# Kernel optimization log

Hardware: AMD Instinct MI355X
Metric: run time of the kernel (lower is better)

## Reference

```python
import jax, jax.numpy as jnp
import numpy as np

EPS = 1e-8

def _center(G):
    # Double-centering: H @ G @ H with H = I - 11^T/n, expressed as mean subtraction.
    # Identical math to the torch H-matmul version, O(n^2) instead of O(n^3).
    row = jnp.mean(G, axis=-1, keepdims=True)
    col = jnp.mean(G, axis=-2, keepdims=True)
    tot = jnp.mean(G, axis=(-2, -1), keepdims=True)
    return G - row - col + tot


def setup_inputs() -> dict:
    key = jax.random.key(0)
    k1, k2 = jax.random.split(key)
    B, L, H, M = 32, 128, 512, 512
    x = jax.random.normal(k1, (B, L, H), dtype=jnp.float32)
    # nn.Embedding.from_pretrained(torch.normal(-0.01, 0.2, (M, L*H)))
    centroid_w = jax.random.normal(k2, (M, L * H), dtype=jnp.float32) * 0.2 - 0.01
    return {"x": x, "centroid_w": centroid_w}


def reference(x, centroid_w):
    B, L, H = x.shape
    M = centroid_w.shape[0]
    cent = centroid_w.reshape(M, L, H)

    # Centered linear Grams
    Cx = _center(jnp.einsum('blh,bkh->blk', x, x))        # (B, L, L)
    Cy = _center(jnp.einsum('mlh,mkh->mlk', cent, cent))  # (M, L, L)

    # linear HSIC: sum over LxL of elementwise product -> (B, M)
    hsic = jnp.einsum('bij,mij->bm', Cx, Cy)
    vx = jnp.sqrt(jnp.sum(Cx * Cx, axis=(1, 2)))  # (B,)  sqrt(HSIC(x,x))
    vy = jnp.sqrt(jnp.sum(Cy * Cy, axis=(1, 2)))  # (M,)  sqrt(HSIC(y,y))
    cka_loss_matrix = -jnp.log(jnp.abs(hsic / (vx[:, None] * vy[None, :])) + EPS)

    idx = jnp.argmax(cka_loss_matrix, axis=-1)  # (B,)
    sel = cent[idx]                              # (B, L, H) gathered centroids

    # Second CKA pass against selected centroids; torch broadcasting makes (B, B)
    Cs = _center(jnp.einsum('blh,bkh->blk', sel, sel))  # (B, L, L)
    hsic2 = jnp.einsum('bij,cij->bc', Cx, Cs)           # (B, B)
    vs = jnp.sqrt(jnp.sum(Cs * Cs, axis=(1, 2)))        # (B,)
    cka_loss = -jnp.log(jnp.mean(jnp.abs(hsic2 / (vx[:, None] * vs[None, :]))) + EPS)

    return cka_loss, cka_loss_matrix, idx
```

## Files before the change

kernel.cpp:

```cpp
#include <hip/hip_runtime.h>
#include <math.h>

#define BB 32
#define LL 128
#define HH 512
#define MM 512
#define NM 544
#define EPSF 1e-8f
#define CPLEN 10240
#define NCH 40

typedef __attribute__((ext_vector_type(8))) short short8b;
typedef __attribute__((ext_vector_type(4))) float f32x4;
typedef __attribute__((ext_vector_type(16))) float f32x16;

#define NWS_CP    0
#define NWS_PART  5570560
#define NWS_NSQ   6225920
#define NWS_HSIC  6226464
#define NWS_IDS   6242848

__device__ __forceinline__ unsigned pack2(unsigned lo, unsigned hi) {
    return (lo >> 16) | (hi & 0xffff0000u);
}

__device__ __forceinline__ void split3(const float4 lo, const float4 hi,
                                       uint4& p0, uint4& p1, uint4& p2) {
    float c[8] = {lo.x, lo.y, lo.z, lo.w, hi.x, hi.y, hi.z, hi.w};
    unsigned h[8], m[8], l[8];
#pragma unroll
    for (int i = 0; i < 8; ++i) {
        h[i] = __float_as_uint(c[i]) & 0xffff0000u;
        const float r1 = c[i] - __uint_as_float(h[i]);
        m[i] = __float_as_uint(r1) & 0xffff0000u;
        l[i] = __float_as_uint(r1 - __uint_as_float(m[i]));
    }
    p0 = make_uint4(pack2(h[0],h[1]), pack2(h[2],h[3]), pack2(h[4],h[5]), pack2(h[6],h[7]));
    p1 = make_uint4(pack2(m[0],m[1]), pack2(m[2],m[3]), pack2(m[4],m[5]), pack2(m[6],m[7]));
    p2 = make_uint4(pack2(l[0],l[1]), pack2(l[2],l[3]), pack2(l[4],l[5]), pack2(l[6],l[7]));
}

__device__ __forceinline__ f32x16 mfma6(f32x16 d, const short8b a[3], const short8b b[3]) {
    d = __builtin_amdgcn_mfma_f32_32x32x16_bf16(a[0], b[0], d, 0, 0, 0);
    d = __builtin_amdgcn_mfma_f32_32x32x16_bf16(a[0], b[1], d, 0, 0, 0);
    d = __builtin_amdgcn_mfma_f32_32x32x16_bf16(a[1], b[0], d, 0, 0, 0);
    d = __builtin_amdgcn_mfma_f32_32x32x16_bf16(a[1], b[1], d, 0, 0, 0);
    d = __builtin_amdgcn_mfma_f32_32x32x16_bf16(a[0], b[2], d, 0, 0, 0);
    d = __builtin_amdgcn_mfma_f32_32x32x16_bf16(a[2], b[0], d, 0, 0, 0);
    return d;
}

__device__ __forceinline__ void ldstrip(const uint4* P, int strip, int lane, short8b f[3]) {
    const int s = lane >> 5;
    const int r = strip * 32 + (lane & 31);
#pragma unroll
    for (int p = 0; p < 3; ++p) {
        uint4 u = P[(p * 2 + s) * 128 + r];
        f[p] = *(const short8b*)&u;
    }
}

__device__ __forceinline__ void tile_sums(f32x16 a, float* S, int i, int j,
                                          bool offd, int lane) {
    const int hi = lane >> 5;
    float rs[16];
#pragma unroll
    for (int q = 0; q < 16; ++q) {
        float s = a[q];
        s += __shfl_xor(s, 1, 64);
        s += __shfl_xor(s, 2, 64);
        s += __shfl_xor(s, 4, 64);
        s += __shfl_xor(s, 8, 64);
        s += __shfl_xor(s, 16, 64);
        rs[q] = s;
    }
    if ((lane & 31) == 0) {
#pragma unroll
        for (int q = 0; q < 16; ++q)
            S[i * 32 + (q & 3) + 8 * (q >> 2) + 4 * hi] += rs[q];
    }
    if (offd) {
        float cs = 0.f;
#pragma unroll
        for (int q = 0; q < 16; ++q) cs += a[q];
        cs += __shfl_xor(cs, 32, 64);
        if (lane < 32) S[j * 32 + lane] += cs;
    }
}

__device__ __forceinline__ float tile_fin(f32x16 a, const float* rmv, float gm,
                                          bool offd, int i, int j,
                                          float* dst, int lane) {
    const int hi = lane >> 5, col = lane & 31;
    const float cj = rmv[j * 32 + col];
    const float sc = offd ? 1.41421356237309505f : 1.f;
    float nsq = 0.f;
#pragma unroll
    for (int c = 0; c < 4; ++c) {
        const float4 ri = *(const float4*)&rmv[i * 32 + c * 8 + hi * 4];
        const float riq[4] = {ri.x, ri.y, ri.z, ri.w};
        f32x4 o;
#pragma unroll
        for (int q = 0; q < 4; ++q) {
            float vq = (a[c * 4 + q] + gm - riq[q] - cj) * sc;
            nsq = fmaf(vq, vq, nsq);
            o[q] = vq;
        }
        *(f32x4*)(dst + (c * 2 + hi) * 128 + col * 4) = o;
    }
    return nsq;
}

__global__ __launch_bounds__(256, 4)
void gram_sym2(const float* __restrict__ x,
               const float* __restrict__ cent,
               float* __restrict__ Cp,
               float* __restrict__ normsq)
{
    __shared__ uint4 planes[2][3][2][128];
    __shared__ float Ssh[4][128];
    __shared__ float rmv[128];
    __shared__ float red[256];
    __shared__ float gmsh;

    const int tid  = threadIdx.x;
    const int lane = tid & 63;
    const int wid  = tid >> 6;
    const int n    = blockIdx.x;
    const float* Amat = (n < BB) ? (x + (size_t)n * LL * HH)
                                 : (cent + (size_t)(n - BB) * LL * HH);

    const int srow  = tid >> 1;
    const int shalf = tid & 1;

    f32x16 a0, a1, a2;
#pragma unroll
    for (int q = 0; q < 16; ++q) { a0[q] = 0.f; a1[q] = 0.f; a2[q] = 0.f; }

    float4 v0 = *(const float4*)(Amat + (size_t)srow * HH + shalf * 8);
    float4 v1 = *(const float4*)(Amat + (size_t)srow * HH + shalf * 8 + 4);

    for (int t = 0; t < 32; ++t) {
        const int pb = t & 1;
        uint4 p0, p1, p2;
        split3(v0, v1, p0, p1, p2);
        uint4* P = &planes[pb][0][0][0];
        const int wbase = shalf * 128 + srow;
        P[0 * 256 + wbase] = p0;
        P[1 * 256 + wbase] = p1;
        P[2 * 256 + wbase] = p2;

        const int kn = (t < 31) ? (t + 1) * 16 : 496;
        v0 = *(const float4*)(Amat + (size_t)srow * HH + kn + shalf * 8);
        v1 = *(const float4*)(Amat + (size_t)srow * HH + kn + shalf * 8 + 4);

        __syncthreads();

        const uint4* Pr = &planes[pb][0][0][0];
        short8b fa[3], fb[3];
        if (wid == 0) {
            ldstrip(Pr, 3, lane, fb);
            ldstrip(Pr, 0, lane, fa); a0 = mfma6(a0, fa, fb);
            ldstrip(Pr, 1, lane, fa); a1 = mfma6(a1, fa, fb);
            ldstrip(Pr, 2, lane, fa); a2 = mfma6(a2, fa, fb);
        } else if (wid == 1) {
            ldstrip(Pr, 3, lane, fa); a0 = mfma6(a0, fa, fa);
            ldstrip(Pr, 2, lane, fb);
            ldstrip(Pr, 0, lane, fa); a1 = mfma6(a1, fa, fb);
            ldstrip(Pr, 1, lane, fa); a2 = mfma6(a2, fa, fb);
        } else if (wid == 2) {
            ldstrip(Pr, 2, lane, fa); a0 = mfma6(a0, fa, fa);
            ldstrip(Pr, 0, lane, fa);
            ldstrip(Pr, 1, lane, fb); a1 = mfma6(a1, fa, fb);
        } else {
            ldstrip(Pr, 0, lane, fa); a0 = mfma6(a0, fa, fa);
            ldstrip(Pr, 1, lane, fa); a1 = mfma6(a1, fa, fa);
        }
    }

    Ssh[wid][lane] = 0.f;
    Ssh[wid][lane + 64] = 0.f;
    if (wid == 0) {
        tile_sums(a0, Ssh[0], 0, 3, true, lane);
        tile_sums(a1, Ssh[0], 1, 3, true, lane);
        tile_sums(a2, Ssh[0], 2, 3, true, lane);
    } else if (wid == 1) {
        tile_sums(a0, Ssh[1], 3, 3, false, lane);
        tile_sums(a1, Ssh[1], 0, 2, true, lane);
        tile_sums(a2, Ssh[1], 1, 2, true, lane);
    } else if (wid == 2) {
        tile_sums(a0, Ssh[2], 2, 2, false, lane);
        tile_sums(a1, Ssh[2], 0, 1, true, lane);
    } else {
        tile_sums(a0, Ssh[3], 0, 0, false, lane);
        tile_sums(a1, Ssh[3], 1, 1, false, lane);
    }
    __syncthreads();

    float Sv = 0.f;
    if (tid < 128) {
        Sv = Ssh[0][tid] + Ssh[1][tid] + Ssh[2][tid] + Ssh[3][tid];
        rmv[tid] = Sv * (1.f / 128.f);
    }
    red[tid] = (tid < 128) ? Sv : 0.f;
    __syncthreads();
    for (int s2 = 128; s2 > 0; s2 >>= 1) {
        if (tid < s2) red[tid] += red[tid + s2];
        __syncthreads();
    }
    if (tid == 0) gmsh = red[0] * (1.f / 16384.f);
    __syncthreads();
    const float gm = gmsh;

    float nsq = 0.f;
    float* dst = Cp + (size_t)n * CPLEN;
    if (wid == 0) {
        nsq += tile_fin(a0, rmv, gm, true, 0, 3, dst + 3 * 1024, lane);
        nsq += tile_fin(a1, rmv, gm, true, 1, 3, dst + 6 * 1024, lane);
        nsq += tile_fin(a2, rmv, gm, true, 2, 3, dst + 8 * 1024, lane);
    } else if (wid == 1) {
        nsq += tile_fin(a0, rmv, gm, false, 3, 3, dst + 9 * 1024, lane);
        nsq += tile_fin(a1, rmv, gm, true, 0, 2, dst + 2 * 1024, lane);
        nsq += tile_fin(a2, rmv, gm, true, 1, 2, dst + 5 * 1024, lane);
    } else if (wid == 2) {
        nsq += tile_fin(a0, rmv, gm, false, 2, 2, dst + 7 * 1024, lane);
        nsq += tile_fin(a1, rmv, gm, true, 0, 1, dst + 1 * 1024, lane);
    } else {
        nsq += tile_fin(a0, rmv, gm, false, 0, 0, dst + 0 * 1024, lane);
        nsq += tile_fin(a1, rmv, gm, false, 1, 1, dst + 4 * 1024, lane);
    }
    __syncthreads();
    red[tid] = nsq;
    __syncthreads();
    for (int s2 = 128; s2 > 0; s2 >>= 1) {
        if (tid < s2) red[tid] += red[tid + s2];
        __syncthreads();
    }
    if (tid == 0) normsq[n] = red[0];
}

__global__ __launch_bounds__(256, 2)
void hsic_partial(const float* __restrict__ Cp, float* __restrict__ part)
{
    __shared__ float cx[32][260];
    __shared__ float red2[256][16];

    const int tid = threadIdx.x;
    const int bx  = blockIdx.x;
    const int mt  = bx / NCH;
    const int kc  = bx % NCH;
    const int k0  = kc * 256;

#pragma unroll
    for (int i = 0; i < 8; ++i) {
        const int idx = i * 1024 + tid * 4;
        const int b = idx >> 8, k = idx & 255;
        *(float4*)&cx[b][k] = *(const float4*)&Cp[(size_t)b * CPLEN + k0 + k];
    }
    __syncthreads();

    const int kq = tid >> 6;
    const int bg = (tid >> 3) & 7;
    const int mg = tid & 7;
    const float* cyBase = Cp + (size_t)(BB + mt * 32 + mg * 4) * CPLEN + k0 + kq * 64;

    float a[4][4];
#pragma unroll
    for (int bi = 0; bi < 4; ++bi)
#pragma unroll
        for (int mi = 0; mi < 4; ++mi) a[bi][mi] = 0.f;

    for (int kk = 0; kk < 16; ++kk) {
        float4 cy[4];
#pragma unroll
        for (int mi = 0; mi < 4; ++mi)
            cy[mi] = *(const float4*)(cyBase + (size_t)mi * CPLEN + kk * 4);
        float4 cxv[4];
#pragma unroll
        for (int bi = 0; bi < 4; ++bi)
            cxv[bi] = *(const float4*)&cx[bg + bi * 8][kq * 64 + kk * 4];
#pragma unroll
        for (int bi = 0; bi < 4; ++bi)
#pragma unroll
            for (int mi = 0; mi < 4; ++mi) {
                a[bi][mi] = fmaf(cxv[bi].x, cy[mi].x, a[bi][mi]);
                a[bi][mi] = fmaf(cxv[bi].y, cy[mi].y, a[bi][mi]);
                a[bi][mi] = fmaf(cxv[bi].z, cy[mi].z, a[bi][mi]);
                a[bi][mi] = fmaf(cxv[bi].w, cy[mi].w, a[bi][mi]);
            }
    }

#pragma unroll
    for (int e = 0; e < 16; ++e) red2[tid][e] = a[e >> 2][e & 3];
    __syncthreads();
    if (tid < 64) {
#pragma unroll
        for (int e = 0; e < 16; ++e) {
            const float s = red2[tid][e] + red2[tid + 64][e] +
                            red2[tid + 128][e] + red2[tid + 192][e];
            const int bi = e >> 2, mi = e & 3;
            const int b = ((tid >> 3) & 7) + bi * 8;
            const int m = mt * 32 + (tid & 7) * 4 + mi;
            part[((size_t)kc * 32 + b) * 512 + m] = s;
        }
    }
}

__global__ __launch_bounds__(256)
void combine_loss(const float* __restrict__ part,
                  const float* __restrict__ normsq,
                  float* __restrict__ hsic,
                  int* __restrict__ ids,
                  float* __restrict__ out)
{
    __shared__ float rv[256];
    __shared__ int   ri[256];
    const int b = blockIdx.x;
    const int tid = threadIdx.x;
    const float vx = sqrtf(normsq[b]);

    float best = -INFINITY; int bm = 0;
    for (int m = tid; m < MM; m += 256) {
        float s = 0.f;
        for (int kc = 0; kc < NCH; ++kc)
            s += part[((size_t)kc * 32 + b) * 512 + m];
        hsic[b * MM + m] = s;
        const float vy = sqrtf(normsq[BB + m]);
        const float loss = -logf(fabsf(s) / (vx * vy) + EPSF);
        out[1 + b * MM + m] = loss;
        if (loss > best) { best = loss; bm = m; }
    }
    rv[tid] = best; ri[tid] = bm;
    __syncthreads();
    for (int s2 = 128; s2 > 0; s2 >>= 1) {
        if (tid < s2) {
            if (rv[tid + s2] > rv[tid] ||
                (rv[tid + s2] == rv[tid] && ri[tid + s2] < ri[tid])) {
                rv[tid] = rv[tid + s2]; ri[tid] = ri[tid + s2];
            }
        }
        __syncthreads();
    }
    if (tid == 0) { ids[b] = ri[0]; out[1 + BB * MM + b] = (float)ri[0]; }
}

__global__ __launch_bounds__(1024)
void scalar_loss(const float* __restrict__ hsic,
                 const float* __restrict__ normsq,
                 const int* __restrict__ ids,
                 float* __restrict__ out)
{
    __shared__ float red[1024];
    const int tid = threadIdx.x;
    const int b = tid >> 5, c = tid & 31;
    const int m = ids[c];
    red[tid] = fabsf(hsic[b * MM + m]) /
               (sqrtf(normsq[b]) * sqrtf(normsq[BB + m]));
    __syncthreads();
    for (int s = 512; s > 0; s >>= 1) {
        if (tid < s) red[tid] += red[tid + s];
        __syncthreads();
    }
    if (tid == 0) out[0] = -logf(red[0] * (1.f / 1024.f) + EPSF);
}

extern "C" void kernel_launch(void* const* d_in, const int* in_sizes, int n_in,
                              void* d_out, int out_size, void* d_ws, size_t ws_size,
                              hipStream_t stream) {
    const float* x    = (const float*)d_in[0];
    const float* cent = (const float*)d_in[1];
    float* out = (float*)d_out;
    float* ws  = (float*)d_ws;

    float* Cp     = ws + NWS_CP;
    float* part   = ws + NWS_PART;
    float* normsq = ws + NWS_NSQ;
    float* hsic   = ws + NWS_HSIC;
    int*   ids    = (int*)(ws + NWS_IDS);

    gram_sym2<<<NM, 256, 0, stream>>>(x, cent, Cp, normsq);
    hsic_partial<<<16 * NCH, 256, 0, stream>>>(Cp, part);
    combine_loss<<<BB, 256, 0, stream>>>(part, normsq, hsic, ids, out);
    scalar_loss<<<1, 1024, 0, stream>>>(hsic, normsq, ids, out);
}
```

Baseline: 89.42 us.

## Split Gram K-dimension across warps with private staging, reduce tiles in LDS

Each of the four warps now owns a quarter of the hidden dimension and computes all ten upper-triangular 32x32 tiles of the Gram matrix for that slice, staging its own split-bf16 planes in private shared memory. This removes the per-step block-wide __syncthreads and the uneven tile-to-warp assignment of the old kernel. The partial tiles are then summed through shared memory in four serialized rounds, and row sums and centering are computed from that buffer. In exchange it needs 160 accumulator registers per lane, which is why launch bounds drop to two blocks per SIMD, and it adds an LDS reduction phase.

Result: slower. 98.05 us (+9.7%).

```diff
diff --git a/kernel.cpp b/kernel.cpp
--- a/kernel.cpp
+++ b/kernel.cpp
@@ -40,85 +40,33 @@
     p2 = make_uint4(pack2(l[0],l[1]), pack2(l[2],l[3]), pack2(l[4],l[5]), pack2(l[6],l[7]));
 }
 
-__device__ __forceinline__ f32x16 mfma6(f32x16 d, const short8b a[3], const short8b b[3]) {
+__device__ __forceinline__ void mfma6(f32x16& d, const short8b a[3], const short8b b[3]) {
     d = __builtin_amdgcn_mfma_f32_32x32x16_bf16(a[0], b[0], d, 0, 0, 0);
     d = __builtin_amdgcn_mfma_f32_32x32x16_bf16(a[0], b[1], d, 0, 0, 0);
     d = __builtin_amdgcn_mfma_f32_32x32x16_bf16(a[1], b[0], d, 0, 0, 0);
     d = __builtin_amdgcn_mfma_f32_32x32x16_bf16(a[1], b[1], d, 0, 0, 0);
     d = __builtin_amdgcn_mfma_f32_32x32x16_bf16(a[0], b[2], d, 0, 0, 0);
     d = __builtin_amdgcn_mfma_f32_32x32x16_bf16(a[2], b[0], d, 0, 0, 0);
-    return d;
-}
-
-__device__ __forceinline__ void ldstrip(const uint4* P, int strip, int lane, short8b f[3]) {
-    const int s = lane >> 5;
-    const int r = strip * 32 + (lane & 31);
-#pragma unroll
-    for (int p = 0; p < 3; ++p) {
-        uint4 u = P[(p * 2 + s) * 128 + r];
-        f[p] = *(const short8b*)&u;
-    }
-}
-
-__device__ __forceinline__ void tile_sums(f32x16 a, float* S, int i, int j,
-                                          bool offd, int lane) {
-    const int hi = lane >> 5;
-    float rs[16];
-#pragma unroll
-    for (int q = 0; q < 16; ++q) {
-        float s = a[q];
-        s += __shfl_xor(s, 1, 64);
-        s += __shfl_xor(s, 2, 64);
-        s += __shfl_xor(s, 4, 64);
-        s += __shfl_xor(s, 8, 64);
-        s += __shfl_xor(s, 16, 64);
-        rs[q] = s;
-    }
-    if ((lane & 31) == 0) {
-#pragma unroll
-        for (int q = 0; q < 16; ++q)
-            S[i * 32 + (q & 3) + 8 * (q >> 2) + 4 * hi] += rs[q];
-    }
-    if (offd) {
-        float cs = 0.f;
-#pragma unroll
-        for (int q = 0; q < 16; ++q) cs += a[q];
-        cs += __shfl_xor(cs, 32, 64);
-        if (lane < 32) S[j * 32 + lane] += cs;
-    }
-}
-
-__device__ __forceinline__ float tile_fin(f32x16 a, const float* rmv, float gm,
-                                          bool offd, int i, int j,
-                                          float* dst, int lane) {
-    const int hi = lane >> 5, col = lane & 31;
-    const float cj = rmv[j * 32 + col];
-    const float sc = offd ? 1.41421356237309505f : 1.f;
-    float nsq = 0.f;
-#pragma unroll
-    for (int c = 0; c < 4; ++c) {
-        const float4 ri = *(const float4*)&rmv[i * 32 + c * 8 + hi * 4];
-        const float riq[4] = {ri.x, ri.y, ri.z, ri.w};
-        f32x4 o;
-#pragma unroll
-        for (int q = 0; q < 4; ++q) {
-            float vq = (a[c * 4 + q] + gm - riq[q] - cj) * sc;
-            nsq = fmaf(vq, vq, nsq);
-            o[q] = vq;
-        }
-        *(f32x4*)(dst + (c * 2 + hi) * 128 + col * 4) = o;
-    }
-    return nsq;
-}
-
-__global__ __launch_bounds__(256, 4)
-void gram_sym2(const float* __restrict__ x,
-               const float* __restrict__ cent,
-               float* __restrict__ Cp,
-               float* __restrict__ normsq)
+}
+
+__device__ __forceinline__ int flatAB(int a, int b) {
+    return ((a >> 3) * 2 + ((a >> 2) & 1)) * 128 + b * 4 + (a & 3);
+}
+
+__device__ __forceinline__ int Tix(int i, int j) {
+    return i * (7 - i) / 2 + j;
+}
+
+__global__ __launch_bounds__(256, 2)
+void gram_nb(const float* __restrict__ x,
+             const float* __restrict__ cent,
+             float* __restrict__ Cp,
+             float* __restrict__ normsq)
 {
-    __shared__ uint4 planes[2][3][2][128];
-    __shared__ float Ssh[4][128];
+    __shared__ union {
+        uint4 stage[4][3][2][128];
+        float buf[12288];
+    } sm;
     __shared__ float rmv[128];
     __shared__ float red[256];
     __shared__ float gmsh;
@@ -130,79 +78,111 @@
     const float* Amat = (n < BB) ? (x + (size_t)n * LL * HH)
                                  : (cent + (size_t)(n - BB) * LL * HH);
 
-    const int srow  = tid >> 1;
-    const int shalf = tid & 1;
-
-    f32x16 a0, a1, a2;
-#pragma unroll
-    for (int q = 0; q < 16; ++q) { a0[q] = 0.f; a1[q] = 0.f; a2[q] = 0.f; }
-
-    float4 v0 = *(const float4*)(Amat + (size_t)srow * HH + shalf * 8);
-    float4 v1 = *(const float4*)(Amat + (size_t)srow * HH + shalf * 8 + 4);
-
-    for (int t = 0; t < 32; ++t) {
-        const int pb = t & 1;
-        uint4 p0, p1, p2;
-        split3(v0, v1, p0, p1, p2);
-        uint4* P = &planes[pb][0][0][0];
-        const int wbase = shalf * 128 + srow;
-        P[0 * 256 + wbase] = p0;
-        P[1 * 256 + wbase] = p1;
-        P[2 * 256 + wbase] = p2;
-
-        const int kn = (t < 31) ? (t + 1) * 16 : 496;
-        v0 = *(const float4*)(Amat + (size_t)srow * HH + kn + shalf * 8);
-        v1 = *(const float4*)(Amat + (size_t)srow * HH + kn + shalf * 8 + 4);
-
-        __syncthreads();
-
-        const uint4* Pr = &planes[pb][0][0][0];
-        short8b fa[3], fb[3];
-        if (wid == 0) {
-            ldstrip(Pr, 3, lane, fb);
-            ldstrip(Pr, 0, lane, fa); a0 = mfma6(a0, fa, fb);
-            ldstrip(Pr, 1, lane, fa); a1 = mfma6(a1, fa, fb);
-            ldstrip(Pr, 2, lane, fa); a2 = mfma6(a2, fa, fb);
-        } else if (wid == 1) {
-            ldstrip(Pr, 3, lane, fa); a0 = mfma6(a0, fa, fa);
-            ldstrip(Pr, 2, lane, fb);
-            ldstrip(Pr, 0, lane, fa); a1 = mfma6(a1, fa, fb);
-            ldstrip(Pr, 1, lane, fa); a2 = mfma6(a2, fa, fb);
-        } else if (wid == 2) {
-            ldstrip(Pr, 2, lane, fa); a0 = mfma6(a0, fa, fa);
-            ldstrip(Pr, 0, lane, fa);
-            ldstrip(Pr, 1, lane, fb); a1 = mfma6(a1, fa, fb);
-        } else {
-            ldstrip(Pr, 0, lane, fa); a0 = mfma6(a0, fa, fa);
-            ldstrip(Pr, 1, lane, fa); a1 = mfma6(a1, fa, fa);
-        }
-    }
-
-    Ssh[wid][lane] = 0.f;
-    Ssh[wid][lane + 64] = 0.f;
-    if (wid == 0) {
-        tile_sums(a0, Ssh[0], 0, 3, true, lane);
-        tile_sums(a1, Ssh[0], 1, 3, true, lane);
-        tile_sums(a2, Ssh[0], 2, 3, true, lane);
-    } else if (wid == 1) {
-        tile_sums(a0, Ssh[1], 3, 3, false, lane);
-        tile_sums(a1, Ssh[1], 0, 2, true, lane);
-        tile_sums(a2, Ssh[1], 1, 2, true, lane);
-    } else if (wid == 2) {
-        tile_sums(a0, Ssh[2], 2, 2, false, lane);
-        tile_sums(a1, Ssh[2], 0, 1, true, lane);
-    } else {
-        tile_sums(a0, Ssh[3], 0, 0, false, lane);
-        tile_sums(a1, Ssh[3], 1, 1, false, lane);
-    }
-    __syncthreads();
-
-    float Sv = 0.f;
+    const int o   = lane & 1;
+    const int r2  = lane >> 1;
+    const int kw  = wid * 128;
+
+    f32x16 acc[10];
+#pragma unroll
+    for (int g = 0; g < 10; ++g)
+#pragma unroll
+        for (int q = 0; q < 16; ++q) acc[g][q] = 0.f;
+
+    uint4* SW = &sm.stage[wid][0][0][0];
+
+    float4 v0[4], v1[4];
+#pragma unroll
+    for (int p = 0; p < 4; ++p) {
+        const float* rp = Amat + (size_t)(32 * p + r2) * HH + kw + o * 8;
+        v0[p] = *(const float4*)rp;
+        v1[p] = *(const float4*)(rp + 4);
+    }
+
+    for (int t = 0; t < 8; ++t) {
+#pragma unroll
+        for (int p = 0; p < 4; ++p) {
+            uint4 q0, q1, q2;
+            split3(v0[p], v1[p], q0, q1, q2);
+            const int r = 32 * p + r2;
+            SW[(0 * 2 + o) * 128 + r] = q0;
+            SW[(1 * 2 + o) * 128 + r] = q1;
+            SW[(2 * 2 + o) * 128 + r] = q2;
+        }
+        const int kn = kw + ((t < 7) ? (t + 1) * 16 : 112);
+#pragma unroll
+        for (int p = 0; p < 4; ++p) {
+            const float* rp = Amat + (size_t)(32 * p + r2) * HH + kn + o * 8;
+            v0[p] = *(const float4*)rp;
+            v1[p] = *(const float4*)(rp + 4);
+        }
+        const int fo = lane >> 5, frr = lane & 31;
+        short8b fr[4][3];
+#pragma unroll
+        for (int s = 0; s < 4; ++s)
+#pragma unroll
+            for (int pl = 0; pl < 3; ++pl) {
+                uint4 u = SW[(pl * 2 + fo) * 128 + s * 32 + frr];
+                fr[s][pl] = *(const short8b*)&u;
+            }
+        mfma6(acc[0], fr[0], fr[0]);
+        mfma6(acc[1], fr[0], fr[1]);
+        mfma6(acc[4], fr[1], fr[1]);
+        mfma6(acc[2], fr[0], fr[2]);
+        mfma6(acc[5], fr[1], fr[2]);
+        mfma6(acc[7], fr[2], fr[2]);
+        mfma6(acc[3], fr[0], fr[3]);
+        mfma6(acc[6], fr[1], fr[3]);
+        mfma6(acc[8], fr[2], fr[3]);
+        mfma6(acc[9], fr[3], fr[3]);
+    }
+
+    __syncthreads();
+
+    const int hi  = lane >> 5, col = lane & 31;
+#pragma unroll
+    for (int w = 0; w < 4; ++w) {
+        if (wid == w) {
+#pragma unroll
+            for (int g = 0; g < 10; ++g)
+#pragma unroll
+                for (int c = 0; c < 4; ++c) {
+                    const int idx = g * 1024 + (c * 2 + hi) * 128 + col * 4;
+                    f32x4 a4;
+                    a4[0] = acc[g][c * 4 + 0];
+                    a4[1] = acc[g][c * 4 + 1];
+                    a4[2] = acc[g][c * 4 + 2];
+                    a4[3] = acc[g][c * 4 + 3];
+                    if (w > 0) {
+                        const f32x4 old = *(const f32x4*)&sm.buf[idx];
+                        a4[0] += old[0]; a4[1] += old[1];
+                        a4[2] += old[2]; a4[3] += old[3];
+                    }
+                    *(f32x4*)&sm.buf[idx] = a4;
+                }
+        }
+        __syncthreads();
+    }
+
+    float s = 0.f;
     if (tid < 128) {
-        Sv = Ssh[0][tid] + Ssh[1][tid] + Ssh[2][tid] + Ssh[3][tid];
-        rmv[tid] = Sv * (1.f / 128.f);
-    }
-    red[tid] = (tid < 128) ? Sv : 0.f;
+        const int i = tid >> 5, ri = tid & 31;
+#pragma unroll
+        for (int j = 0; j < 4; ++j) {
+            if (j >= i) {
+                const int g = Tix(i, j);
+#pragma unroll
+                for (int b = 0; b < 32; ++b)
+                    s += sm.buf[g * 1024 + flatAB(ri, b)];
+            } else {
+                const int g = Tix(j, i);
+#pragma unroll
+                for (int a = 0; a < 32; ++a)
+                    s += sm.buf[g * 1024 + flatAB(a, ri)];
+            }
+        }
+        rmv[tid] = s * (1.f / 128.f);
+    }
+    red[tid] = (tid < 128) ? s : 0.f;
     __syncthreads();
     for (int s2 = 128; s2 > 0; s2 >>= 1) {
         if (tid < s2) red[tid] += red[tid + s2];
@@ -212,22 +192,29 @@
     __syncthreads();
     const float gm = gmsh;
 
+    const int b  = tid & 31;
+    const int c2 = tid >> 5;
+    const int ar = (c2 >> 1) * 8 + (c2 & 1) * 4;
     float nsq = 0.f;
-    float* dst = Cp + (size_t)n * CPLEN;
-    if (wid == 0) {
-        nsq += tile_fin(a0, rmv, gm, true, 0, 3, dst + 3 * 1024, lane);
-        nsq += tile_fin(a1, rmv, gm, true, 1, 3, dst + 6 * 1024, lane);
-        nsq += tile_fin(a2, rmv, gm, true, 2, 3, dst + 8 * 1024, lane);
-    } else if (wid == 1) {
-        nsq += tile_fin(a0, rmv, gm, false, 3, 3, dst + 9 * 1024, lane);
-        nsq += tile_fin(a1, rmv, gm, true, 0, 2, dst + 2 * 1024, lane);
-        nsq += tile_fin(a2, rmv, gm, true, 1, 2, dst + 5 * 1024, lane);
-    } else if (wid == 2) {
-        nsq += tile_fin(a0, rmv, gm, false, 2, 2, dst + 7 * 1024, lane);
-        nsq += tile_fin(a1, rmv, gm, true, 0, 1, dst + 1 * 1024, lane);
-    } else {
-        nsq += tile_fin(a0, rmv, gm, false, 0, 0, dst + 0 * 1024, lane);
-        nsq += tile_fin(a1, rmv, gm, false, 1, 1, dst + 4 * 1024, lane);
+    float* dstn = Cp + (size_t)n * CPLEN;
+    static const int TI[10] = {0,0,0,0,1,1,1,2,2,3};
+    static const int TJ[10] = {0,1,2,3,1,2,3,2,3,3};
+#pragma unroll
+    for (int g = 0; g < 10; ++g) {
+        const int i = TI[g], j = TJ[g];
+        const float sc = (i == j) ? 1.f : 1.41421356237309505f;
+        const f32x4 vv = *(const f32x4*)&sm.buf[g * 1024 + tid * 4];
+        const float4 rr = *(const float4*)&rmv[i * 32 + ar];
+        const float riq[4] = {rr.x, rr.y, rr.z, rr.w};
+        const float cj = rmv[j * 32 + b];
+        f32x4 ov;
+#pragma unroll
+        for (int q = 0; q < 4; ++q) {
+            const float val = (vv[q] + gm - riq[q] - cj) * sc;
+            nsq = fmaf(val, val, nsq);
+            ov[q] = val;
+        }
+        *(f32x4*)(dstn + g * 1024 + tid * 4) = ov;
     }
     __syncthreads();
     red[tid] = nsq;
@@ -378,7 +365,7 @@
     float* hsic   = ws + NWS_HSIC;
     int*   ids    = (int*)(ws + NWS_IDS);
 
-    gram_sym2<<<NM, 256, 0, stream>>>(x, cent, Cp, normsq);
+    gram_nb<<<NM, 256, 0, stream>>>(x, cent, Cp, normsq);
     hsic_partial<<<16 * NCH, 256, 0, stream>>>(Cp, part);
     combine_loss<<<BB, 256, 0, stream>>>(part, normsq, hsic, ids, out);
     scalar_loss<<<1, 1024, 0, stream>>>(hsic, normsq, ids, out);
```

## Load gram strips per wave directly and center only x grams

Applied to the files above, without the earlier changes.

Each wave now loads its own row strips straight from global memory into registers, splits them into bf16x3 parts and issues MFMAs with no LDS staging and no per-step block barriers. Centroid grams are stored uncentered. Their centered squared norm comes from row sums (sum of squares minus a row-sum correction plus a total-sum term), and a small new kernel centers only the 32 x grams. This relies on a centered Cx making the HSIC inner product the same whether or not Cy is centered. In exchange, strips shared by several waves are loaded and split several times, and occupancy bounds drop from 4 to 2 blocks. The norm formula also subtracts large terms, which can lose float precision.

Result: slower. 122.6 us (+37.1%).

```diff
diff --git a/kernel.cpp b/kernel.cpp
--- a/kernel.cpp
+++ b/kernel.cpp
@@ -9,6 +9,7 @@
 #define EPSF 1e-8f
 #define CPLEN 10240
 #define NCH 40
+#define R2C 1.41421356237309505f
 
 typedef __attribute__((ext_vector_type(8))) short short8b;
 typedef __attribute__((ext_vector_type(4))) float f32x4;
@@ -19,6 +20,7 @@
 #define NWS_NSQ   6225920
 #define NWS_HSIC  6226464
 #define NWS_IDS   6242848
+#define NWS_U     6242880
 
 __device__ __forceinline__ unsigned pack2(unsigned lo, unsigned hi) {
     return (lo >> 16) | (hi & 0xffff0000u);
@@ -40,24 +42,17 @@
     p2 = make_uint4(pack2(l[0],l[1]), pack2(l[2],l[3]), pack2(l[4],l[5]), pack2(l[6],l[7]));
 }
 
-__device__ __forceinline__ f32x16 mfma6(f32x16 d, const short8b a[3], const short8b b[3]) {
+__device__ __forceinline__ void mfma6(f32x16& d, const short8b a[3], const short8b b[3]) {
     d = __builtin_amdgcn_mfma_f32_32x32x16_bf16(a[0], b[0], d, 0, 0, 0);
     d = __builtin_amdgcn_mfma_f32_32x32x16_bf16(a[0], b[1], d, 0, 0, 0);
     d = __builtin_amdgcn_mfma_f32_32x32x16_bf16(a[1], b[0], d, 0, 0, 0);
     d = __builtin_amdgcn_mfma_f32_32x32x16_bf16(a[1], b[1], d, 0, 0, 0);
     d = __builtin_amdgcn_mfma_f32_32x32x16_bf16(a[0], b[2], d, 0, 0, 0);
     d = __builtin_amdgcn_mfma_f32_32x32x16_bf16(a[2], b[0], d, 0, 0, 0);
-    return d;
-}
-
-__device__ __forceinline__ void ldstrip(const uint4* P, int strip, int lane, short8b f[3]) {
-    const int s = lane >> 5;
-    const int r = strip * 32 + (lane & 31);
-#pragma unroll
-    for (int p = 0; p < 3; ++p) {
-        uint4 u = P[(p * 2 + s) * 128 + r];
-        f[p] = *(const short8b*)&u;
-    }
+}
+
+__device__ __forceinline__ constexpr int Tix(int i, int j) {
+    return i * (7 - i) / 2 + j;
 }
 
 __device__ __forceinline__ void tile_sums(f32x16 a, float* S, int i, int j,
@@ -88,155 +83,211 @@
     }
 }
 
-__device__ __forceinline__ float tile_fin(f32x16 a, const float* rmv, float gm,
-                                          bool offd, int i, int j,
-                                          float* dst, int lane) {
-    const int hi = lane >> 5, col = lane & 31;
-    const float cj = rmv[j * 32 + col];
-    const float sc = offd ? 1.41421356237309505f : 1.f;
+__device__ __forceinline__ float tile_store(const f32x16& a, float* dst,
+                                            bool offd, int lane) {
+    const int oct = lane >> 5, col = lane & 31;
+    const float sc = offd ? R2C : 1.f;
     float nsq = 0.f;
 #pragma unroll
     for (int c = 0; c < 4; ++c) {
-        const float4 ri = *(const float4*)&rmv[i * 32 + c * 8 + hi * 4];
-        const float riq[4] = {ri.x, ri.y, ri.z, ri.w};
         f32x4 o;
 #pragma unroll
         for (int q = 0; q < 4; ++q) {
-            float vq = (a[c * 4 + q] + gm - riq[q] - cj) * sc;
-            nsq = fmaf(vq, vq, nsq);
-            o[q] = vq;
-        }
-        *(f32x4*)(dst + (c * 2 + hi) * 128 + col * 4) = o;
+            const float v = a[c * 4 + q] * sc;
+            nsq = fmaf(v, v, nsq);
+            o[q] = v;
+        }
+        *(f32x4*)(dst + (c * 2 + oct) * 128 + col * 4) = o;
     }
     return nsq;
 }
 
-__global__ __launch_bounds__(256, 4)
-void gram_sym2(const float* __restrict__ x,
-               const float* __restrict__ cent,
-               float* __restrict__ Cp,
-               float* __restrict__ normsq)
-{
-    __shared__ uint4 planes[2][3][2][128];
+template<int NS, int NT, int S0, int S1, int S2, int S3,
+         int A0, int B0, int A1, int B1, int A2, int B2>
+__device__ __forceinline__ float wave_gram(const float* __restrict__ Amat,
+                                           float* __restrict__ Sslice,
+                                           float* __restrict__ dstn,
+                                           int lane)
+{
+    const int r31 = lane & 31, oct = lane >> 5;
+    const int SS[4] = {S0, S1, S2, S3};
+
+    Sslice[lane] = 0.f;
+    Sslice[lane + 64] = 0.f;
+
+    const float* base[4];
+#pragma unroll
+    for (int s = 0; s < NS; ++s)
+        base[s] = Amat + (size_t)(SS[s] * 32 + r31) * HH + oct * 8;
+
+    f32x16 t0, t1, t2;
+#pragma unroll
+    for (int q = 0; q < 16; ++q) { t0[q] = 0.f; t1[q] = 0.f; t2[q] = 0.f; }
+
+    float4 cur[4][2], nxt[4][2];
+#pragma unroll
+    for (int s = 0; s < NS; ++s) {
+        cur[s][0] = *(const float4*)(base[s]);
+        cur[s][1] = *(const float4*)(base[s] + 4);
+    }
+
+#pragma unroll 1
+    for (int tt = 0; tt < 16; ++tt) {
+#pragma unroll
+        for (int s = 0; s < NS; ++s) {
+            const float* p = base[s] + (2 * tt + 1) * 16;
+            nxt[s][0] = *(const float4*)p;
+            nxt[s][1] = *(const float4*)(p + 4);
+        }
+        {
+            short8b fr[4][3];
+#pragma unroll
+            for (int s = 0; s < NS; ++s) {
+                uint4 u0, u1, u2;
+                split3(cur[s][0], cur[s][1], u0, u1, u2);
+                fr[s][0] = *(short8b*)&u0;
+                fr[s][1] = *(short8b*)&u1;
+                fr[s][2] = *(short8b*)&u2;
+            }
+            mfma6(t0, fr[A0], fr[B0]);
+            if (NT > 1) mfma6(t1, fr[A1], fr[B1]);
+            if (NT > 2) mfma6(t2, fr[A2], fr[B2]);
+        }
+        if (tt < 15) {
+#pragma unroll
+            for (int s = 0; s < NS; ++s) {
+                const float* p = base[s] + (2 * tt + 2) * 16;
+                cur[s][0] = *(const float4*)p;
+                cur[s][1] = *(const float4*)(p + 4);
+            }
+        }
+        {
+            short8b fr[4][3];
+#pragma unroll
+            for (int s = 0; s < NS; ++s) {
+                uint4 u0, u1, u2;
+                split3(nxt[s][0], nxt[s][1], u0, u1, u2);
+                fr[s][0] = *(short8b*)&u0;
+                fr[s][1] = *(short8b*)&u1;
+                fr[s][2] = *(short8b*)&u2;
+            }
+            mfma6(t0, fr[A0], fr[B0]);
+            if (NT > 1) mfma6(t1, fr[A1], fr[B1]);
+            if (NT > 2) mfma6(t2, fr[A2], fr[B2]);
+        }
+    }
+
+    tile_sums(t0, Sslice, SS[A0], SS[B0], SS[A0] != SS[B0], lane);
+    if (NT > 1) tile_sums(t1, Sslice, SS[A1], SS[B1], SS[A1] != SS[B1], lane);
+    if (NT > 2) tile_sums(t2, Sslice, SS[A2], SS[B2], SS[A2] != SS[B2], lane);
+
+    float nsq = tile_store(t0, dstn + Tix(SS[A0], SS[B0]) * 1024,
+                           SS[A0] != SS[B0], lane);
+    if (NT > 1) nsq += tile_store(t1, dstn + Tix(SS[A1], SS[B1]) * 1024,
+                                  SS[A1] != SS[B1], lane);
+    if (NT > 2) nsq += tile_store(t2, dstn + Tix(SS[A2], SS[B2]) * 1024,
+                                  SS[A2] != SS[B2], lane);
+    return nsq;
+}
+
+__global__ __launch_bounds__(256, 2)
+void gram_direct(const float* __restrict__ x,
+                 const float* __restrict__ cent,
+                 float* __restrict__ Cp,
+                 float* __restrict__ normsq,
+                 float* __restrict__ uws)
+{
     __shared__ float Ssh[4][128];
-    __shared__ float rmv[128];
     __shared__ float red[256];
-    __shared__ float gmsh;
-
-    const int tid  = threadIdx.x;
-    const int lane = tid & 63;
-    const int wid  = tid >> 6;
-    const int n    = blockIdx.x;
+    __shared__ float sS, sUsq;
+
+    const int tid = threadIdx.x, lane = tid & 63, wid = tid >> 6;
+    const int n = blockIdx.x;
     const float* Amat = (n < BB) ? (x + (size_t)n * LL * HH)
                                  : (cent + (size_t)(n - BB) * LL * HH);
-
-    const int srow  = tid >> 1;
-    const int shalf = tid & 1;
-
-    f32x16 a0, a1, a2;
-#pragma unroll
-    for (int q = 0; q < 16; ++q) { a0[q] = 0.f; a1[q] = 0.f; a2[q] = 0.f; }
-
-    float4 v0 = *(const float4*)(Amat + (size_t)srow * HH + shalf * 8);
-    float4 v1 = *(const float4*)(Amat + (size_t)srow * HH + shalf * 8 + 4);
-
-    for (int t = 0; t < 32; ++t) {
-        const int pb = t & 1;
-        uint4 p0, p1, p2;
-        split3(v0, v1, p0, p1, p2);
-        uint4* P = &planes[pb][0][0][0];
-        const int wbase = shalf * 128 + srow;
-        P[0 * 256 + wbase] = p0;
-        P[1 * 256 + wbase] = p1;
-        P[2 * 256 + wbase] = p2;
-
-        const int kn = (t < 31) ? (t + 1) * 16 : 496;
-        v0 = *(const float4*)(Amat + (size_t)srow * HH + kn + shalf * 8);
-        v1 = *(const float4*)(Amat + (size_t)srow * HH + kn + shalf * 8 + 4);
-
-        __syncthreads();
-
-        const uint4* Pr = &planes[pb][0][0][0];
-        short8b fa[3], fb[3];
-        if (wid == 0) {
-            ldstrip(Pr, 3, lane, fb);
-            ldstrip(Pr, 0, lane, fa); a0 = mfma6(a0, fa, fb);
-            ldstrip(Pr, 1, lane, fa); a1 = mfma6(a1, fa, fb);
-            ldstrip(Pr, 2, lane, fa); a2 = mfma6(a2, fa, fb);
-        } else if (wid == 1) {
-            ldstrip(Pr, 3, lane, fa); a0 = mfma6(a0, fa, fa);
-            ldstrip(Pr, 2, lane, fb);
-            ldstrip(Pr, 0, lane, fa); a1 = mfma6(a1, fa, fb);
-            ldstrip(Pr, 1, lane, fa); a2 = mfma6(a2, fa, fb);
-        } else if (wid == 2) {
-            ldstrip(Pr, 2, lane, fa); a0 = mfma6(a0, fa, fa);
-            ldstrip(Pr, 0, lane, fa);
-            ldstrip(Pr, 1, lane, fb); a1 = mfma6(a1, fa, fb);
-        } else {
-            ldstrip(Pr, 0, lane, fa); a0 = mfma6(a0, fa, fa);
-            ldstrip(Pr, 1, lane, fa); a1 = mfma6(a1, fa, fa);
-        }
-    }
-
-    Ssh[wid][lane] = 0.f;
-    Ssh[wid][lane + 64] = 0.f;
-    if (wid == 0) {
-        tile_sums(a0, Ssh[0], 0, 3, true, lane);
-        tile_sums(a1, Ssh[0], 1, 3, true, lane);
-        tile_sums(a2, Ssh[0], 2, 3, true, lane);
-    } else if (wid == 1) {
-        tile_sums(a0, Ssh[1], 3, 3, false, lane);
-        tile_sums(a1, Ssh[1], 0, 2, true, lane);
-        tile_sums(a2, Ssh[1], 1, 2, true, lane);
-    } else if (wid == 2) {
-        tile_sums(a0, Ssh[2], 2, 2, false, lane);
-        tile_sums(a1, Ssh[2], 0, 1, true, lane);
-    } else {
-        tile_sums(a0, Ssh[3], 0, 0, false, lane);
-        tile_sums(a1, Ssh[3], 1, 1, false, lane);
-    }
-    __syncthreads();
-
-    float Sv = 0.f;
+    float* dstn = Cp + (size_t)n * CPLEN;
+
+    float nsq;
+    if (wid == 0)      nsq = wave_gram<4,3, 0,1,2,3, 0,3, 1,3, 2,3>(Amat, Ssh[0], dstn, lane);
+    else if (wid == 1) nsq = wave_gram<4,3, 3,2,0,1, 0,0, 2,1, 3,1>(Amat, Ssh[1], dstn, lane);
+    else if (wid == 2) nsq = wave_gram<3,2, 2,0,1,0, 0,0, 1,2, 0,0>(Amat, Ssh[2], dstn, lane);
+    else               nsq = wave_gram<2,2, 0,1,0,0, 0,0, 1,1, 0,0>(Amat, Ssh[3], dstn, lane);
+    __syncthreads();
+
+    float u = 0.f;
     if (tid < 128) {
-        Sv = Ssh[0][tid] + Ssh[1][tid] + Ssh[2][tid] + Ssh[3][tid];
-        rmv[tid] = Sv * (1.f / 128.f);
-    }
-    red[tid] = (tid < 128) ? Sv : 0.f;
+        u = Ssh[0][tid] + Ssh[1][tid] + Ssh[2][tid] + Ssh[3][tid];
+        uws[(size_t)n * 128 + tid] = u;
+    }
+    red[tid] = (tid < 128) ? u : 0.f;
     __syncthreads();
     for (int s2 = 128; s2 > 0; s2 >>= 1) {
         if (tid < s2) red[tid] += red[tid + s2];
         __syncthreads();
     }
-    if (tid == 0) gmsh = red[0] * (1.f / 16384.f);
-    __syncthreads();
-    const float gm = gmsh;
-
-    float nsq = 0.f;
-    float* dst = Cp + (size_t)n * CPLEN;
-    if (wid == 0) {
-        nsq += tile_fin(a0, rmv, gm, true, 0, 3, dst + 3 * 1024, lane);
-        nsq += tile_fin(a1, rmv, gm, true, 1, 3, dst + 6 * 1024, lane);
-        nsq += tile_fin(a2, rmv, gm, true, 2, 3, dst + 8 * 1024, lane);
-    } else if (wid == 1) {
-        nsq += tile_fin(a0, rmv, gm, false, 3, 3, dst + 9 * 1024, lane);
-        nsq += tile_fin(a1, rmv, gm, true, 0, 2, dst + 2 * 1024, lane);
-        nsq += tile_fin(a2, rmv, gm, true, 1, 2, dst + 5 * 1024, lane);
-    } else if (wid == 2) {
-        nsq += tile_fin(a0, rmv, gm, false, 2, 2, dst + 7 * 1024, lane);
-        nsq += tile_fin(a1, rmv, gm, true, 0, 1, dst + 1 * 1024, lane);
-    } else {
-        nsq += tile_fin(a0, rmv, gm, false, 0, 0, dst + 0 * 1024, lane);
-        nsq += tile_fin(a1, rmv, gm, false, 1, 1, dst + 4 * 1024, lane);
-    }
-    __syncthreads();
-    red[tid] = nsq;
+    if (tid == 0) sS = red[0];
+    __syncthreads();
+    red[tid] = (tid < 128) ? u * u : 0.f;
     __syncthreads();
     for (int s2 = 128; s2 > 0; s2 >>= 1) {
         if (tid < s2) red[tid] += red[tid + s2];
         __syncthreads();
     }
-    if (tid == 0) normsq[n] = red[0];
+    if (tid == 0) sUsq = red[0];
+    __syncthreads();
+    red[tid] = nsq;
+    __syncthreads();
+    for (int s2 = 128; s2 > 0; s2 >>= 1) {
+        if (tid < s2) red[tid] += red[tid + s2];
+        __syncthreads();
+    }
+    if (tid == 0) {
+        const float sv = sS * (1.f / 128.f);
+        normsq[n] = red[0] - sUsq * (1.f / 64.f) + sv * sv;
+    }
+}
+
+__global__ __launch_bounds__(256)
+void center_x(float* __restrict__ Cp, const float* __restrict__ uws)
+{
+    __shared__ float rmv[128];
+    __shared__ float red[128];
+    __shared__ float gmsh;
+
+    const int n = blockIdx.x, tid = threadIdx.x;
+    if (tid < 128) {
+        const float u = uws[(size_t)n * 128 + tid];
+        rmv[tid] = u * (1.f / 128.f);
+        red[tid] = u;
+    }
+    __syncthreads();
+    for (int s2 = 64; s2 > 0; s2 >>= 1) {
+        if (tid < s2) red[tid] += red[tid + s2];
+        __syncthreads();
+    }
+    if (tid == 0) gmsh = red[0] * (1.f / 16384.f);
+    __syncthreads();
+    const float gm = gmsh;
+
+    float* base = Cp + (size_t)n * CPLEN;
+    static const int TI[10] = {0,0,0,0,1,1,1,2,2,3};
+    static const int TJ[10] = {0,1,2,3,1,2,3,2,3,3};
+#pragma unroll
+    for (int it = 0; it < 10; ++it) {
+        const int u4  = it * 256 + tid;
+        const int rem = u4 & 255;
+        const int c2  = rem >> 5;
+        const int col = rem & 31;
+        const int ab  = (c2 >> 1) * 8 + (c2 & 1) * 4;
+        const int i = TI[it], j = TJ[it];
+        const float sc = (i == j) ? 1.f : R2C;
+        const float cj = rmv[j * 32 + col];
+        f32x4 v = *(f32x4*)(base + (size_t)u4 * 4);
+#pragma unroll
+        for (int q = 0; q < 4; ++q)
+            v[q] -= sc * (rmv[i * 32 + ab + q] + cj - gm);
+        *(f32x4*)(base + (size_t)u4 * 4) = v;
+    }
 }
 
 __global__ __launch_bounds__(256, 2)
@@ -377,8 +428,10 @@
     float* normsq = ws + NWS_NSQ;
     float* hsic   = ws + NWS_HSIC;
     int*   ids    = (int*)(ws + NWS_IDS);
-
-    gram_sym2<<<NM, 256, 0, stream>>>(x, cent, Cp, normsq);
+    float* uws    = ws + NWS_U;
+
+    gram_direct<<<NM, 256, 0, stream>>>(x, cent, Cp, normsq, uws);
+    center_x<<<BB, 256, 0, stream>>>(Cp, uws);
     hsic_partial<<<16 * NCH, 256, 0, stream>>>(Cp, part);
     combine_loss<<<BB, 256, 0, stream>>>(part, normsq, hsic, ids, out);
     scalar_loss<<<1, 1024, 0, stream>>>(hsic, normsq, ids, out);
```

## Restructure Gram kernel to stage fp32 chunks in swizzled LDS and split at read

Applied to the files above, without the earlier changes.

Replaces the per-16-column double-buffered bf16 plane staging with 64-column fp32 chunks held in an XOR-swizzled LDS buffer. Each wave now reads its fragments and does the three-way bf16 split itself, and the 10 symmetric tiles are reassigned across waves. This cuts the number of barrier-separated K steps from 32 to 8 and moves the split work off the store path, aimed at lowering sync and global-load overhead. In exchange, split3 now runs redundantly for every fragment read, LDS use grows to 32KB, occupancy drops to 3 blocks, and nothing overlaps loading the next chunk with the MFMAs.

After: 117.2 us. 1.31x slower.

```diff
diff --git a/kernel.cpp b/kernel.cpp
--- a/kernel.cpp
+++ b/kernel.cpp
@@ -9,6 +9,7 @@
 #define EPSF 1e-8f
 #define CPLEN 10240
 #define NCH 40
+#define R2C 1.41421356237309505f
 
 typedef __attribute__((ext_vector_type(8))) short short8b;
 typedef __attribute__((ext_vector_type(4))) float f32x4;
@@ -40,24 +41,13 @@
     p2 = make_uint4(pack2(l[0],l[1]), pack2(l[2],l[3]), pack2(l[4],l[5]), pack2(l[6],l[7]));
 }
 
-__device__ __forceinline__ f32x16 mfma6(f32x16 d, const short8b a[3], const short8b b[3]) {
+__device__ __forceinline__ void mfma6(f32x16& d, const short8b a[3], const short8b b[3]) {
     d = __builtin_amdgcn_mfma_f32_32x32x16_bf16(a[0], b[0], d, 0, 0, 0);
     d = __builtin_amdgcn_mfma_f32_32x32x16_bf16(a[0], b[1], d, 0, 0, 0);
     d = __builtin_amdgcn_mfma_f32_32x32x16_bf16(a[1], b[0], d, 0, 0, 0);
     d = __builtin_amdgcn_mfma_f32_32x32x16_bf16(a[1], b[1], d, 0, 0, 0);
     d = __builtin_amdgcn_mfma_f32_32x32x16_bf16(a[0], b[2], d, 0, 0, 0);
     d = __builtin_amdgcn_mfma_f32_32x32x16_bf16(a[2], b[0], d, 0, 0, 0);
-    return d;
-}
-
-__device__ __forceinline__ void ldstrip(const uint4* P, int strip, int lane, short8b f[3]) {
-    const int s = lane >> 5;
-    const int r = strip * 32 + (lane & 31);
-#pragma unroll
-    for (int p = 0; p < 3; ++p) {
-        uint4 u = P[(p * 2 + s) * 128 + r];
-        f[p] = *(const short8b*)&u;
-    }
 }
 
 __device__ __forceinline__ void tile_sums(f32x16 a, float* S, int i, int j,
@@ -93,7 +83,7 @@
                                           float* dst, int lane) {
     const int hi = lane >> 5, col = lane & 31;
     const float cj = rmv[j * 32 + col];
-    const float sc = offd ? 1.41421356237309505f : 1.f;
+    const float sc = offd ? R2C : 1.f;
     float nsq = 0.f;
 #pragma unroll
     for (int c = 0; c < 4; ++c) {
@@ -111,89 +101,100 @@
     return nsq;
 }
 
-__global__ __launch_bounds__(256, 4)
-void gram_sym2(const float* __restrict__ x,
-               const float* __restrict__ cent,
-               float* __restrict__ Cp,
-               float* __restrict__ normsq)
-{
-    __shared__ uint4 planes[2][3][2][128];
+__device__ __forceinline__ void frag_rd(const float* fbuf, int r, int u,
+                                        short8b f[3]) {
+    const int sw = (r & 7) << 4;
+    const float4 lo = *(const float4*)((const char*)fbuf + (r * 256 + ((u * 16) ^ sw)));
+    const float4 hi = *(const float4*)((const char*)fbuf + (r * 256 + (((u + 1) * 16) ^ sw)));
+    uint4 p0, p1, p2;
+    split3(lo, hi, p0, p1, p2);
+    f[0] = *(short8b*)&p0;
+    f[1] = *(short8b*)&p1;
+    f[2] = *(short8b*)&p2;
+}
+
+template<int NS, int NT, int S0, int S1, int S2,
+         int A0, int B0, int A1, int B1, int A2, int B2>
+__device__ __forceinline__ void mfma_phase(const float* fbuf, int lane,
+                                           f32x16& t0, f32x16& t1, f32x16& t2)
+{
+    const int o = lane >> 5, r31 = lane & 31;
+    const int SS[3] = {S0, S1, S2};
+#pragma unroll
+    for (int t = 0; t < 4; ++t) {
+        short8b fr[3][3];
+#pragma unroll
+        for (int s = 0; s < NS; ++s)
+            frag_rd(fbuf, SS[s] * 32 + r31, t * 4 + o * 2, fr[s]);
+        mfma6(t0, fr[A0], fr[B0]);
+        if (NT > 1) mfma6(t1, fr[A1], fr[B1]);
+        if (NT > 2) mfma6(t2, fr[A2], fr[B2]);
+    }
+}
+
+__global__ __launch_bounds__(256, 3)
+void gram_ph(const float* __restrict__ x,
+             const float* __restrict__ cent,
+             float* __restrict__ Cp,
+             float* __restrict__ normsq)
+{
+    __shared__ __align__(16) float fbuf[8192];
     __shared__ float Ssh[4][128];
     __shared__ float rmv[128];
     __shared__ float red[256];
     __shared__ float gmsh;
 
-    const int tid  = threadIdx.x;
-    const int lane = tid & 63;
-    const int wid  = tid >> 6;
-    const int n    = blockIdx.x;
+    const int tid = threadIdx.x, lane = tid & 63, wid = tid >> 6;
+    const int n = blockIdx.x;
     const float* Amat = (n < BB) ? (x + (size_t)n * LL * HH)
                                  : (cent + (size_t)(n - BB) * LL * HH);
 
-    const int srow  = tid >> 1;
-    const int shalf = tid & 1;
-
-    f32x16 a0, a1, a2;
-#pragma unroll
-    for (int q = 0; q < 16; ++q) { a0[q] = 0.f; a1[q] = 0.f; a2[q] = 0.f; }
-
-    float4 v0 = *(const float4*)(Amat + (size_t)srow * HH + shalf * 8);
-    float4 v1 = *(const float4*)(Amat + (size_t)srow * HH + shalf * 8 + 4);
-
-    for (int t = 0; t < 32; ++t) {
-        const int pb = t & 1;
-        uint4 p0, p1, p2;
-        split3(v0, v1, p0, p1, p2);
-        uint4* P = &planes[pb][0][0][0];
-        const int wbase = shalf * 128 + srow;
-        P[0 * 256 + wbase] = p0;
-        P[1 * 256 + wbase] = p1;
-        P[2 * 256 + wbase] = p2;
-
-        const int kn = (t < 31) ? (t + 1) * 16 : 496;
-        v0 = *(const float4*)(Amat + (size_t)srow * HH + kn + shalf * 8);
-        v1 = *(const float4*)(Amat + (size_t)srow * HH + kn + shalf * 8 + 4);
-
-        __syncthreads();
-
-        const uint4* Pr = &planes[pb][0][0][0];
-        short8b fa[3], fb[3];
-        if (wid == 0) {
-            ldstrip(Pr, 3, lane, fb);
-            ldstrip(Pr, 0, lane, fa); a0 = mfma6(a0, fa, fb);
-            ldstrip(Pr, 1, lane, fa); a1 = mfma6(a1, fa, fb);
-            ldstrip(Pr, 2, lane, fa); a2 = mfma6(a2, fa, fb);
-        } else if (wid == 1) {
-            ldstrip(Pr, 3, lane, fa); a0 = mfma6(a0, fa, fa);
-            ldstrip(Pr, 2, lane, fb);
-            ldstrip(Pr, 0, lane, fa); a1 = mfma6(a1, fa, fb);
-            ldstrip(Pr, 1, lane, fa); a2 = mfma6(a2, fa, fb);
-        } else if (wid == 2) {
-            ldstrip(Pr, 2, lane, fa); a0 = mfma6(a0, fa, fa);
-            ldstrip(Pr, 0, lane, fa);
-            ldstrip(Pr, 1, lane, fb); a1 = mfma6(a1, fa, fb);
-        } else {
-            ldstrip(Pr, 0, lane, fa); a0 = mfma6(a0, fa, fa);
-            ldstrip(Pr, 1, lane, fa); a1 = mfma6(a1, fa, fa);
+    const int lrow = lane >> 4;
+    const int lu   = lane & 15;
+    const int rbase = wid * 32 + lrow;
+
+    f32x16 t0, t1, t2;
+#pragma unroll
+    for (int q = 0; q < 16; ++q) { t0[q] = 0.f; t1[q] = 0.f; t2[q] = 0.f; }
+
+#pragma unroll 1
+    for (int p = 0; p < 8; ++p) {
+        float4 st[8];
+#pragma unroll
+        for (int i = 0; i < 8; ++i)
+            st[i] = *(const float4*)(Amat + (size_t)(rbase + i * 4) * HH +
+                                     p * 64 + lu * 4);
+        __syncthreads();
+#pragma unroll
+        for (int i = 0; i < 8; ++i) {
+            const int r = rbase + i * 4;
+            *(float4*)((char*)fbuf + (r * 256 + ((lu * 16) ^ ((r & 7) << 4)))) = st[i];
+        }
+        __syncthreads();
+        switch (wid) {
+            case 0:  mfma_phase<2,3, 0,1,0, 0,0, 0,1, 1,1>(fbuf, lane, t0, t1, t2); break;
+            case 1:  mfma_phase<2,3, 2,3,0, 0,0, 0,1, 1,1>(fbuf, lane, t0, t1, t2); break;
+            case 2:  mfma_phase<3,2, 0,2,3, 0,1, 0,2, 0,0>(fbuf, lane, t0, t1, t2); break;
+            default: mfma_phase<3,2, 1,2,3, 0,1, 0,2, 0,0>(fbuf, lane, t0, t1, t2); break;
         }
     }
 
     Ssh[wid][lane] = 0.f;
     Ssh[wid][lane + 64] = 0.f;
     if (wid == 0) {
-        tile_sums(a0, Ssh[0], 0, 3, true, lane);
-        tile_sums(a1, Ssh[0], 1, 3, true, lane);
-        tile_sums(a2, Ssh[0], 2, 3, true, lane);
+        tile_sums(t0, Ssh[0], 0, 0, false, lane);
+        tile_sums(t1, Ssh[0], 0, 1, true,  lane);
+        tile_sums(t2, Ssh[0], 1, 1, false, lane);
     } else if (wid == 1) {
-        tile_sums(a0, Ssh[1], 3, 3, false, lane);
-        tile_sums(a1, Ssh[1], 0, 2, true, lane);
-        tile_sums(a2, Ssh[1], 1, 2, true, lane);
+        tile_sums(t0, Ssh[1], 2, 2, false, lane);
+        tile_sums(t1, Ssh[1], 2, 3, true,  lane);
+        tile_sums(t2, Ssh[1], 3, 3, false, lane);
     } else if (wid == 2) {
-        tile_sums(a0, Ssh[2], 2, 2, false, lane);
-        tile_sums(a1, Ssh[2], 0, 1, true, lane);
+        tile_sums(t0, Ssh[2], 0, 2, true, lane);
+        tile_sums(t1, Ssh[2], 0, 3, true, lane);
     } else {
-        tile_sums(a0, Ssh[3], 0, 0, false, lane);
-        tile_sums(a1, Ssh[3], 1, 1, false, lane);
+        tile_sums(t0, Ssh[3], 1, 2, true, lane);
+        tile_sums(t1, Ssh[3], 1, 3, true, lane);
     }
     __syncthreads();
 
@@ -215,19 +216,19 @@
     float nsq = 0.f;
     float* dst = Cp + (size_t)n * CPLEN;
     if (wid == 0) {
-        nsq += tile_fin(a0, rmv, gm, true, 0, 3, dst + 3 * 1024, lane);
-        nsq += tile_fin(a1, rmv, gm, true, 1, 3, dst + 6 * 1024, lane);
-        nsq += tile_fin(a2, rmv, gm, true, 2, 3, dst + 8 * 1024, lane);
+        nsq += tile_fin(t0, rmv, gm, false, 0, 0, dst + 0 * 1024, lane);
+        nsq += tile_fin(t1, rmv, gm, true,  0, 1, dst + 1 * 1024, lane);
+        nsq += tile_fin(t2, rmv, gm, false, 1, 1, dst + 4 * 1024, lane);
     } else if (wid == 1) {
-        nsq += tile_fin(a0, rmv, gm, false, 3, 3, dst + 9 * 1024, lane);
-        nsq += tile_fin(a1, rmv, gm, true, 0, 2, dst + 2 * 1024, lane);
-        nsq += tile_fin(a2, rmv, gm, true, 1, 2, dst + 5 * 1024, lane);
+        nsq += tile_fin(t0, rmv, gm, false, 2, 2, dst + 7 * 1024, lane);
+        nsq += tile_fin(t1, rmv, gm, true,  2, 3, dst + 8 * 1024, lane);
+        nsq += tile_fin(t2, rmv, gm, false, 3, 3, dst + 9 * 1024, lane);
     } else if (wid == 2) {
-        nsq += tile_fin(a0, rmv, gm, false, 2, 2, dst + 7 * 1024, lane);
-        nsq += tile_fin(a1, rmv, gm, true, 0, 1, dst + 1 * 1024, lane);
+        nsq += tile_fin(t0, rmv, gm, true, 0, 2, dst + 2 * 1024, lane);
+        nsq += tile_fin(t1, rmv, gm, true, 0, 3, dst + 3 * 1024, lane);
     } else {
-        nsq += tile_fin(a0, rmv, gm, false, 0, 0, dst + 0 * 1024, lane);
-        nsq += tile_fin(a1, rmv, gm, false, 1, 1, dst + 4 * 1024, lane);
+        nsq += tile_fin(t0, rmv, gm, true, 1, 2, dst + 5 * 1024, lane);
+        nsq += tile_fin(t1, rmv, gm, true, 1, 3, dst + 6 * 1024, lane);
     }
     __syncthreads();
     red[tid] = nsq;
@@ -378,7 +379,7 @@
     float* hsic   = ws + NWS_HSIC;
     int*   ids    = (int*)(ws + NWS_IDS);
 
-    gram_sym2<<<NM, 256, 0, stream>>>(x, cent, Cp, normsq);
+    gram_ph<<<NM, 256, 0, stream>>>(x, cent, Cp, normsq);
     hsic_partial<<<16 * NCH, 256, 0, stream>>>(Cp, part);
     combine_loss<<<BB, 256, 0, stream>>>(part, normsq, hsic, ids, out);
     scalar_loss<<<1, 1024, 0, stream>>>(hsic, normsq, ids, out);
```
